# Kernel tuning notes

Measured on AMD Instinct MI355X. Metric: run time of the kernel, lower is better.

## Reference

```python
import jax, jax.numpy as jnp
import numpy as np

N_NODES = 50000
N_EDGES = 800000
IN_DIM, HID_DIM, OUT_DIM = 128, 64, 64
NEG_SLOPE = 0.2


def setup_inputs() -> dict:
    key = jax.random.key(0)
    ks = jax.random.split(key, 9)
    return {
        "x": jax.random.normal(ks[0], (N_NODES, IN_DIM), dtype=jnp.float32),
        "edge_index": jax.random.randint(ks[1], (2, N_EDGES), 0, N_NODES, dtype=jnp.int64),
        "W1": jax.random.normal(ks[2], (IN_DIM, HID_DIM), dtype=jnp.float32) * 0.1,
        "a1_src": jax.random.normal(ks[3], (HID_DIM,), dtype=jnp.float32) * 0.1,
        "a1_dst": jax.random.normal(ks[4], (HID_DIM,), dtype=jnp.float32) * 0.1,
        "b1": jnp.zeros((HID_DIM,), dtype=jnp.float32),
        "W2": jax.random.normal(ks[5], (HID_DIM, OUT_DIM), dtype=jnp.float32) * 0.1,
        "a2_src": jax.random.normal(ks[6], (OUT_DIM,), dtype=jnp.float32) * 0.1,
        "a2_dst": jax.random.normal(ks[7], (OUT_DIM,), dtype=jnp.float32) * 0.1,
        "b2": jnp.zeros((OUT_DIM,), dtype=jnp.float32),
    }


def gat_conv(x, src, dst, W, a_src, a_dst, b, n_nodes):
    """Single-head GATConv (PyG semantics, self-loops already appended)."""
    h = x @ W                               # [N, D]
    s_src = h @ a_src                       # [N]
    s_dst = h @ a_dst                       # [N]
    e = s_src[src] + s_dst[dst]             # [E] edge logits
    e = jnp.where(e >= 0, e, NEG_SLOPE * e)  # leaky_relu(0.2)
    # softmax over incoming edges of each destination node (numerically stable)
    m = jax.ops.segment_max(e, dst, num_segments=n_nodes)   # [N]
    e = jnp.exp(e - m[dst])
    denom = jax.ops.segment_sum(e, dst, num_segments=n_nodes)
    alpha = e / denom[dst]                  # [E]
    out = jax.ops.segment_sum(alpha[:, None] * h[src], dst, num_segments=n_nodes)
    return out + b


def reference(x, edge_index, W1, a1_src, a1_dst, b1, W2, a2_src, a2_dst, b2):
    n = x.shape[0]
    loop = jnp.arange(n, dtype=edge_index.dtype)
    src = jnp.concatenate([edge_index[0], loop])  # add self loops (PyG default)
    dst = jnp.concatenate([edge_index[1], loop])
    h = jax.nn.relu(gat_conv(x, src, dst, W1, a1_src, a1_dst, b1, n))
    out = gat_conv(h, src, dst, W2, a2_src, a2_dst, b2, n)
    return out
```

## Files before the change

kernel.cpp:

```cpp
#include <hip/hip_runtime.h>
#include <hip/hip_fp16.h>

#define N_NODES 50000
#define N_EDGES 800000
#define NEG_SLOPE 0.2f
#define NBKT 196
#define EBLK 200
#define CHUNK 4000
#define GEMM_BLOCKS 782

__device__ __forceinline__ float leaky(float x) { return x >= 0.f ? x : NEG_SLOPE * x; }
__device__ __forceinline__ float readlane_f(float v, int i) {
    return __uint_as_float(__builtin_amdgcn_readlane(__float_as_uint(v), i));
}
__device__ __forceinline__ unsigned enc_f(float f) {
    unsigned u = __float_as_uint(f);
    return (int)u < 0 ? ~u : (u | 0x80000000u);
}
__device__ __forceinline__ float dec_f(unsigned e) {
    return __uint_as_float((int)e < 0 ? (e & 0x7FFFFFFFu) : ~e);
}

template <int K>
__device__ __forceinline__ void gemm_body(
    const float* __restrict__ x, const float* __restrict__ W,
    const float* __restrict__ a_src, const float* __restrict__ a_dst,
    __half* __restrict__ h, float* __restrict__ s_src, float* __restrict__ s_dst,
    float* __restrict__ bmax, unsigned* __restrict__ gmax_enc, int n)
{
    constexpr int BK = 32;
    __shared__ float Wl[BK][64];
    __shared__ float xt[BK][68];
    __shared__ float asl[64], adl[64];
    __shared__ float wm[4];

    int tid = threadIdx.x;
    if (tid < 64) { asl[tid] = a_src[tid]; adl[tid] = a_dst[tid]; }
    int tx = tid & 15, ty = tid >> 4;
    int row0 = blockIdx.x * 64;

    float acc[4][4] = {};

    for (int k0 = 0; k0 < K; k0 += BK) {
        __syncthreads();
        {
            const float4* Wg = (const float4*)&W[(size_t)k0 * 64];
            float4* Ws = (float4*)&Wl[0][0];
            Ws[tid]       = Wg[tid];
            Ws[tid + 256] = Wg[tid + 256];
        }
        #pragma unroll
        for (int it = 0; it < 2; ++it) {
            int idx = tid + it * 256;
            int r = idx >> 3, kq = idx & 7;
            int grow = row0 + r;
            float4 v = (grow < n) ? *(const float4*)&x[(size_t)grow * K + k0 + kq * 4]
                                  : make_float4(0.f, 0.f, 0.f, 0.f);
            xt[kq * 4 + 0][r] = v.x;
            xt[kq * 4 + 1][r] = v.y;
            xt[kq * 4 + 2][r] = v.z;
            xt[kq * 4 + 3][r] = v.w;
        }
        __syncthreads();

        #pragma unroll
        for (int kk = 0; kk < BK; ++kk) {
            float4 wv = *(const float4*)&Wl[kk][tx * 4];
            float4 xv = *(const float4*)&xt[kk][ty * 4];
            acc[0][0] += xv.x * wv.x; acc[0][1] += xv.x * wv.y; acc[0][2] += xv.x * wv.z; acc[0][3] += xv.x * wv.w;
            acc[1][0] += xv.y * wv.x; acc[1][1] += xv.y * wv.y; acc[1][2] += xv.y * wv.z; acc[1][3] += xv.y * wv.w;
            acc[2][0] += xv.z * wv.x; acc[2][1] += xv.z * wv.y; acc[2][2] += xv.z * wv.z; acc[2][3] += xv.z * wv.w;
            acc[3][0] += xv.w * wv.x; acc[3][1] += xv.w * wv.y; acc[3][2] += xv.w * wv.z; acc[3][3] += xv.w * wv.w;
        }
    }

    float wmax = -INFINITY;
    #pragma unroll
    for (int i = 0; i < 4; ++i) {
        int grow = row0 + ty * 4 + i;
        if (grow < n) {
            __half2 p0 = __floats2half2_rn(acc[i][0], acc[i][1]);
            __half2 p1 = __floats2half2_rn(acc[i][2], acc[i][3]);
            uint2 pk = make_uint2(*(unsigned*)&p0, *(unsigned*)&p1);
            *(uint2*)&h[(size_t)grow * 64 + tx * 4] = pk;
        }
        float s1 = acc[i][0] * asl[tx*4+0] + acc[i][1] * asl[tx*4+1]
                 + acc[i][2] * asl[tx*4+2] + acc[i][3] * asl[tx*4+3];
        float s2 = acc[i][0] * adl[tx*4+0] + acc[i][1] * adl[tx*4+1]
                 + acc[i][2] * adl[tx*4+2] + acc[i][3] * adl[tx*4+3];
        #pragma unroll
        for (int m = 1; m < 16; m <<= 1) {
            s1 += __shfl_xor(s1, m, 64);
            s2 += __shfl_xor(s2, m, 64);
        }
        if (grow < n) wmax = fmaxf(wmax, s1);
        if (tx == 0 && grow < n) { s_src[grow] = s1; s_dst[grow] = s2; }
    }
    wmax = fmaxf(wmax, __shfl_xor(wmax, 16, 64));
    wmax = fmaxf(wmax, __shfl_xor(wmax, 32, 64));
    if ((tid & 63) == 0) wm[tid >> 6] = wmax;
    __syncthreads();
    if (tid == 0) {
        float bm = fmaxf(fmaxf(wm[0], wm[1]), fmaxf(wm[2], wm[3]));
        if (bmax) bmax[blockIdx.x] = bm;
        else      atomicMax(gmax_enc, enc_f(bm));
    }
}

template <int K>
__global__ __launch_bounds__(256) void fused_gemm_p1(
    const float* __restrict__ x, const float* __restrict__ W,
    const float* __restrict__ a_src, const float* __restrict__ a_dst,
    __half* __restrict__ h, float* __restrict__ s_src, float* __restrict__ s_dst,
    float* __restrict__ bmax,
    const int* __restrict__ dst_, int* __restrict__ cnt, int n)
{
    if (blockIdx.x >= GEMM_BLOCKS) {
        __shared__ int bins[NBKT];
        int tid = threadIdx.x, b = blockIdx.x - GEMM_BLOCKS;
        if (tid < NBKT) bins[tid] = 0;
        __syncthreads();
        int e0 = b * CHUNK;
        for (int e = e0 + tid; e < e0 + CHUNK; e += 256)
            atomicAdd(&bins[dst_[e] >> 8], 1);
        __syncthreads();
        if (tid < NBKT) cnt[b * NBKT + tid] = bins[tid];
        return;
    }
    gemm_body<K>(x, W, a_src, a_dst, h, s_src, s_dst, bmax, nullptr, n);
}

template <int K>
__global__ __launch_bounds__(256) void gat_gemm_kernel(
    const float* __restrict__ x, const float* __restrict__ W,
    const float* __restrict__ a_src, const float* __restrict__ a_dst,
    __half* __restrict__ h, float* __restrict__ s_src, float* __restrict__ s_dst,
    unsigned* __restrict__ gmax_enc, int n)
{
    gemm_body<K>(x, W, a_src, a_dst, h, s_src, s_dst, nullptr, gmax_enc, n);
}

__global__ __launch_bounds__(256) void p23_fused(
    const int* __restrict__ cnt, int* __restrict__ btot,
    const float* __restrict__ bmax, unsigned* __restrict__ gmaxu,
    const int* __restrict__ src, const int* __restrict__ dst,
    unsigned* __restrict__ bkted)
{
    __shared__ int tmp[256];
    __shared__ int boffL[NBKT];
    __shared__ float fm[4];
    int b = blockIdx.x, tid = threadIdx.x;

    int total = 0, myoff = 0;
    if (tid < NBKT) {
        for (int bp = 0; bp < EBLK; ++bp) {
            int v = cnt[bp * NBKT + tid];
            total += v;
            if (bp < b) myoff += v;
        }
    }
    tmp[tid] = (tid < NBKT) ? total : 0;
    __syncthreads();
    for (int off = 1; off < 256; off <<= 1) {
        int a = (tid >= off) ? tmp[tid - off] : 0;
        __syncthreads();
        tmp[tid] += a;
        __syncthreads();
    }
    if (tid < NBKT) {
        int base = tmp[tid] - total;
        boffL[tid] = base + myoff;
        if (b == 0) btot[tid] = total;
    }
    __syncthreads();

    int e0 = b * CHUNK;
    for (int e = e0 + tid; e < e0 + CHUNK; e += 256) {
        int d = dst[e], s = src[e];
        int pos = atomicAdd(&boffL[d >> 8], 1);
        bkted[pos] = ((unsigned)(d & 255) << 16) | (unsigned)s;
    }

    if (b == 0) {
        float m = -INFINITY;
        for (int i = tid; i < GEMM_BLOCKS; i += 256) m = fmaxf(m, bmax[i]);
        #pragma unroll
        for (int off = 32; off; off >>= 1) m = fmaxf(m, __shfl_xor(m, off, 64));
        if ((tid & 63) == 0) fm[tid >> 6] = m;
        __syncthreads();
        if (tid == 0) {
            gmaxu[0] = enc_f(fmaxf(fmaxf(fm[0], fm[1]), fmaxf(fm[2], fm[3])));
            gmaxu[1] = 0;
        }
    }
}

__global__ __launch_bounds__(256) void p4_csr(
    const unsigned* __restrict__ bkted, const int* __restrict__ btot,
    int* __restrict__ row_off, int* __restrict__ csr_src)
{
    __shared__ int tmp[256];
    __shared__ int cur[256];
    __shared__ int s_beg, s_end;
    int j = blockIdx.x, tid = threadIdx.x;
    int v = (tid < NBKT) ? btot[tid] : 0;
    tmp[tid] = v; __syncthreads();
    for (int off = 1; off < 256; off <<= 1) {
        int a = (tid >= off) ? tmp[tid - off] : 0;
        __syncthreads();
        tmp[tid] += a;
        __syncthreads();
    }
    if (tid == j) { s_beg = tmp[tid] - v; s_end = tmp[tid]; }
    cur[tid] = 0;
    __syncthreads();
    int beg = s_beg, end = s_end;

    for (int e = beg + tid; e < end; e += 256)
        atomicAdd(&cur[bkted[e] >> 16], 1);
    __syncthreads();
    int c = cur[tid];
    tmp[tid] = c; __syncthreads();
    for (int off = 1; off < 256; off <<= 1) {
        int a = (tid >= off) ? tmp[tid - off] : 0;
        __syncthreads();
        tmp[tid] += a;
        __syncthreads();
    }
    int offx = tmp[tid] - c;
    int node = j * 256 + tid;
    if (node < N_NODES) row_off[node] = beg + offx;
    if (node == 0) row_off[N_NODES] = N_EDGES;
    __syncthreads();
    cur[tid] = offx;
    __syncthreads();
    for (int e = beg + tid; e < end; e += 256) {
        unsigned u = bkted[e];
        int pos = beg + atomicAdd(&cur[u >> 16], 1);
        csr_src[pos] = (int)(u & 0xFFFFu);
    }
}

template <bool RELU>
__global__ __launch_bounds__(256) void gat_node_kernel(
    const int* __restrict__ row_off, const int* __restrict__ csr_src,
    const float* __restrict__ s_src, const float* __restrict__ s_dst,
    const __half* __restrict__ h, const float* __restrict__ b,
    const unsigned* __restrict__ gmax_enc, float* __restrict__ out, int n)
{
    int row = blockIdx.x * 4 + (threadIdx.x >> 6);
    int lane = threadIdx.x & 63;
    if (row >= n) return;

    int beg = row_off[row], end = row_off[row + 1];
    int deg = end - beg;
    float sd = s_dst[row];
    float m = leaky(dec_f(*gmax_enc) + sd);
    float s_self = s_src[row];
    float hself = __half2float(h[(size_t)row * 64 + lane]);
    float wself = __expf(leaky(s_self + sd) - m);

    if (deg <= 32) {
        int mysrc = row;
        if (lane < deg) mysrc = csr_src[beg + lane];
        float my_s = s_src[mysrc];
        float hv[32];
        #pragma unroll
        for (int j = 0; j < 32; ++j) {
            int s = __builtin_amdgcn_readlane(mysrc, j);
            hv[j] = __half2float(h[(size_t)s * 64 + lane]);
        }
        float mylogit = (lane < deg) ? leaky(my_s + sd) : -INFINITY;
        float w64 = __expf(mylogit - m);
        float den = w64;
        #pragma unroll
        for (int off = 32; off; off >>= 1)
            den += __shfl_xor(den, off, 64);
        den += wself;

        float acc = wself * hself;
        #pragma unroll
        for (int j = 0; j < 32; ++j)
            acc += readlane_f(w64, j) * hv[j];

        float v = acc / den + b[lane];
        if (RELU) v = fmaxf(v, 0.f);
        out[(size_t)row * 64 + lane] = v;
        return;
    }

    int   mysrc   = row;
    float mylogit = -INFINITY;
    if (lane < deg) {
        mysrc = csr_src[beg + lane];
        mylogit = leaky(s_src[mysrc] + sd);
    }
    float w64 = __expf(mylogit - m);
    float den = w64;
    #pragma unroll
    for (int off = 32; off; off >>= 1)
        den += __shfl_xor(den, off, 64);
    den += wself;

    float acc = wself * hself;
    int d0 = deg < 64 ? deg : 64;
    int nb = (d0 + 15) & ~15;
    for (int i = 0; i < nb; i += 16) {
        float hv[16];
        #pragma unroll
        for (int j = 0; j < 16; ++j) {
            int s = __builtin_amdgcn_readlane(mysrc, i + j);
            hv[j] = __half2float(h[(size_t)s * 64 + lane]);
        }
        #pragma unroll
        for (int j = 0; j < 16; ++j)
            acc += readlane_f(w64, i + j) * hv[j];
    }
    for (int e = beg + 64; e < end; ++e) {
        int s = csr_src[e];
        float w = __expf(leaky(s_src[s] + sd) - m);
        den += w;
        acc += w * __half2float(h[(size_t)s * 64 + lane]);
    }

    float v = acc / den + b[lane];
    if (RELU) v = fmaxf(v, 0.f);
    out[(size_t)row * 64 + lane] = v;
}

extern "C" void kernel_launch(void* const* d_in, const int* in_sizes, int n_in,
                              void* d_out, int out_size, void* d_ws, size_t ws_size,
                              hipStream_t stream) {
    const float* x   = (const float*)d_in[0];
    const int*   ei  = (const int*)d_in[1];
    const float* W1  = (const float*)d_in[2];
    const float* a1s = (const float*)d_in[3];
    const float* a1d = (const float*)d_in[4];
    const float* b1  = (const float*)d_in[5];
    const float* W2  = (const float*)d_in[6];
    const float* a2s = (const float*)d_in[7];
    const float* a2d = (const float*)d_in[8];
    const float* b2  = (const float*)d_in[9];
    float* out = (float*)d_out;

    const int* src = ei;
    const int* dst = ei + N_EDGES;

    char* p = (char*)d_ws;
    __half* h   = (__half*)p;           p += (size_t)N_NODES * 64 * 2;
    float* ssrc = (float*)p;            p += (size_t)N_NODES * 4;
    float* sdst = (float*)p;            p += (size_t)N_NODES * 4;
    int* row_off = (int*)p;             p += (size_t)(N_NODES + 1) * 4;
    unsigned* gmaxu = (unsigned*)p;     p += 4 * 4;
    float* bmax = (float*)p;            p += 1024 * 4;
    int* csr_src = (int*)p;             p += (size_t)N_EDGES * 4;
    int* cnt     = (int*)p;             p += (size_t)EBLK * NBKT * 4;
    int* btot    = (int*)p;             p += (size_t)NBKT * 4;
    unsigned* bkted = (unsigned*)p;     p += (size_t)N_EDGES * 4;

    dim3 blk(256);
    int node_blocks = (N_NODES + 3) / 4;

    fused_gemm_p1<128><<<GEMM_BLOCKS + EBLK, blk, 0, stream>>>(
        x, W1, a1s, a1d, h, ssrc, sdst, bmax, dst, cnt, N_NODES);
    p23_fused<<<EBLK, blk, 0, stream>>>(cnt, btot, bmax, gmaxu, src, dst, bkted);
    p4_csr<<<NBKT, blk, 0, stream>>>(bkted, btot, row_off, csr_src);
    gat_node_kernel<true><<<node_blocks, blk, 0, stream>>>(
        row_off, csr_src, ssrc, sdst, h, b1, gmaxu + 0, out, N_NODES);
    gat_gemm_kernel<64><<<GEMM_BLOCKS, blk, 0, stream>>>(
        out, W2, a2s, a2d, h, ssrc, sdst, gmaxu + 1, N_NODES);
    gat_node_kernel<false><<<node_blocks, blk, 0, stream>>>(
        row_off, csr_src, ssrc, sdst, h, b2, gmaxu + 1, out, N_NODES);
}
```

Measured before the change: 125.8 us.

## Fuse layer-1 aggregation with layer-2 GEMM in one node kernel

Merges the first GAT aggregation kernel with the second layer's dense transform. Each wavefront computes its aggregated row, applies ReLU, and multiplies by W2 held in shared memory using readlane broadcasts. It then writes h2, the attention scores and the block max directly, so the fp32 hidden activation never goes to global memory and one launch is removed. It also adds a 16-neighbour gather path for low-degree rows. The cost is separate h2/score buffers and a 64-step serial readlane matvec per row, along with a 16 KB W2 load per block.

Result: slower. 229.8 us (+82.7%).

```diff
diff --git a/kernel.cpp b/kernel.cpp
--- a/kernel.cpp
+++ b/kernel.cpp
@@ -21,12 +21,29 @@
     return __uint_as_float((int)e < 0 ? (e & 0x7FFFFFFFu) : ~e);
 }
 
+template <int NL>
+__device__ __forceinline__ float salvo(int mysrc, float w64,
+                                       const __half* __restrict__ h,
+                                       int lane, float acc)
+{
+    float hv[NL];
+    #pragma unroll
+    for (int j = 0; j < NL; ++j) {
+        int s = __builtin_amdgcn_readlane(mysrc, j);
+        hv[j] = __half2float(h[(size_t)s * 64 + lane]);
+    }
+    #pragma unroll
+    for (int j = 0; j < NL; ++j)
+        acc += readlane_f(w64, j) * hv[j];
+    return acc;
+}
+
 template <int K>
 __device__ __forceinline__ void gemm_body(
     const float* __restrict__ x, const float* __restrict__ W,
     const float* __restrict__ a_src, const float* __restrict__ a_dst,
     __half* __restrict__ h, float* __restrict__ s_src, float* __restrict__ s_dst,
-    float* __restrict__ bmax, unsigned* __restrict__ gmax_enc, int n)
+    float* __restrict__ bmax, int n)
 {
     constexpr int BK = 32;
     __shared__ float Wl[BK][64];
@@ -100,11 +117,8 @@
     wmax = fmaxf(wmax, __shfl_xor(wmax, 32, 64));
     if ((tid & 63) == 0) wm[tid >> 6] = wmax;
     __syncthreads();
-    if (tid == 0) {
-        float bm = fmaxf(fmaxf(wm[0], wm[1]), fmaxf(wm[2], wm[3]));
-        if (bmax) bmax[blockIdx.x] = bm;
-        else      atomicMax(gmax_enc, enc_f(bm));
-    }
+    if (tid == 0)
+        bmax[blockIdx.x] = fmaxf(fmaxf(wm[0], wm[1]), fmaxf(wm[2], wm[3]));
 }
 
 template <int K>
@@ -127,17 +141,7 @@
         if (tid < NBKT) cnt[b * NBKT + tid] = bins[tid];
         return;
     }
-    gemm_body<K>(x, W, a_src, a_dst, h, s_src, s_dst, bmax, nullptr, n);
-}
-
-template <int K>
-__global__ __launch_bounds__(256) void gat_gemm_kernel(
-    const float* __restrict__ x, const float* __restrict__ W,
-    const float* __restrict__ a_src, const float* __restrict__ a_dst,
-    __half* __restrict__ h, float* __restrict__ s_src, float* __restrict__ s_dst,
-    unsigned* __restrict__ gmax_enc, int n)
-{
-    gemm_body<K>(x, W, a_src, a_dst, h, s_src, s_dst, nullptr, gmax_enc, n);
+    gemm_body<K>(x, W, a_src, a_dst, h, s_src, s_dst, bmax, n);
 }
 
 __global__ __launch_bounds__(256) void p23_fused(
@@ -241,53 +245,19 @@
     }
 }
 
-template <bool RELU>
-__global__ __launch_bounds__(256) void gat_node_kernel(
+__device__ __forceinline__ float aggregate_row(
+    int row, int lane,
     const int* __restrict__ row_off, const int* __restrict__ csr_src,
     const float* __restrict__ s_src, const float* __restrict__ s_dst,
-    const __half* __restrict__ h, const float* __restrict__ b,
-    const unsigned* __restrict__ gmax_enc, float* __restrict__ out, int n)
-{
-    int row = blockIdx.x * 4 + (threadIdx.x >> 6);
-    int lane = threadIdx.x & 63;
-    if (row >= n) return;
-
+    const __half* __restrict__ h, const float* __restrict__ bvec,
+    float m_base)
+{
     int beg = row_off[row], end = row_off[row + 1];
     int deg = end - beg;
     float sd = s_dst[row];
-    float m = leaky(dec_f(*gmax_enc) + sd);
-    float s_self = s_src[row];
+    float m = leaky(m_base + sd);
     float hself = __half2float(h[(size_t)row * 64 + lane]);
-    float wself = __expf(leaky(s_self + sd) - m);
-
-    if (deg <= 32) {
-        int mysrc = row;
-        if (lane < deg) mysrc = csr_src[beg + lane];
-        float my_s = s_src[mysrc];
-        float hv[32];
-        #pragma unroll
-        for (int j = 0; j < 32; ++j) {
-            int s = __builtin_amdgcn_readlane(mysrc, j);
-            hv[j] = __half2float(h[(size_t)s * 64 + lane]);
-        }
-        float mylogit = (lane < deg) ? leaky(my_s + sd) : -INFINITY;
-        float w64 = __expf(mylogit - m);
-        float den = w64;
-        #pragma unroll
-        for (int off = 32; off; off >>= 1)
-            den += __shfl_xor(den, off, 64);
-        den += wself;
-
-        float acc = wself * hself;
-        #pragma unroll
-        for (int j = 0; j < 32; ++j)
-            acc += readlane_f(w64, j) * hv[j];
-
-        float v = acc / den + b[lane];
-        if (RELU) v = fmaxf(v, 0.f);
-        out[(size_t)row * 64 + lane] = v;
-        return;
-    }
+    float wself = __expf(leaky(s_src[row] + sd) - m);
 
     int   mysrc   = row;
     float mylogit = -INFINITY;
@@ -303,28 +273,116 @@
     den += wself;
 
     float acc = wself * hself;
-    int d0 = deg < 64 ? deg : 64;
-    int nb = (d0 + 15) & ~15;
-    for (int i = 0; i < nb; i += 16) {
-        float hv[16];
+
+    if (deg <= 16) {
+        acc = salvo<16>(mysrc, w64, h, lane, acc);
+    } else if (deg <= 32) {
+        acc = salvo<32>(mysrc, w64, h, lane, acc);
+    } else {
+        int d0 = deg < 64 ? deg : 64;
+        int nb = (d0 + 15) & ~15;
+        for (int i = 0; i < nb; i += 16) {
+            float hv[16];
+            #pragma unroll
+            for (int j = 0; j < 16; ++j) {
+                int s = __builtin_amdgcn_readlane(mysrc, i + j);
+                hv[j] = __half2float(h[(size_t)s * 64 + lane]);
+            }
+            #pragma unroll
+            for (int j = 0; j < 16; ++j)
+                acc += readlane_f(w64, i + j) * hv[j];
+        }
+        for (int e = beg + 64; e < end; ++e) {
+            int s = csr_src[e];
+            float w = __expf(leaky(s_src[s] + sd) - m);
+            den += w;
+            acc += w * __half2float(h[(size_t)s * 64 + lane]);
+        }
+    }
+    return acc / den + bvec[lane];
+}
+
+__global__ __launch_bounds__(256) void node1_gemm2_kernel(
+    const int* __restrict__ row_off, const int* __restrict__ csr_src,
+    const float* __restrict__ s_src, const float* __restrict__ s_dst,
+    const __half* __restrict__ h, const float* __restrict__ b1,
+    const float* __restrict__ W2,
+    const float* __restrict__ a2s, const float* __restrict__ a2d,
+    const unsigned* __restrict__ gmax1_enc, unsigned* __restrict__ gmax2_enc,
+    __half* __restrict__ h2, float* __restrict__ s_src2, float* __restrict__ s_dst2,
+    int n)
+{
+    __shared__ float W2l[64][64];
+    __shared__ float b1l[64], a2sl[64], a2dl[64];
+    __shared__ float wm[4];
+
+    int tid = threadIdx.x;
+    {
+        const float4* Wg = (const float4*)W2;
+        float4* Ws = (float4*)&W2l[0][0];
         #pragma unroll
-        for (int j = 0; j < 16; ++j) {
-            int s = __builtin_amdgcn_readlane(mysrc, i + j);
-            hv[j] = __half2float(h[(size_t)s * 64 + lane]);
-        }
-        #pragma unroll
-        for (int j = 0; j < 16; ++j)
-            acc += readlane_f(w64, i + j) * hv[j];
-    }
-    for (int e = beg + 64; e < end; ++e) {
-        int s = csr_src[e];
-        float w = __expf(leaky(s_src[s] + sd) - m);
-        den += w;
-        acc += w * __half2float(h[(size_t)s * 64 + lane]);
-    }
-
-    float v = acc / den + b[lane];
-    if (RELU) v = fmaxf(v, 0.f);
+        for (int it = 0; it < 4; ++it)
+            Ws[tid + it * 256] = Wg[tid + it * 256];
+        if (tid < 64) { b1l[tid] = b1[tid]; a2sl[tid] = a2s[tid]; a2dl[tid] = a2d[tid]; }
+    }
+    __syncthreads();
+
+    int row = blockIdx.x * 4 + (tid >> 6);
+    int lane = tid & 63;
+    float m_base = dec_f(*gmax1_enc);
+
+    float v = 0.f;
+    if (row < n) {
+        v = aggregate_row(row, lane, row_off, csr_src, s_src, s_dst, h, b1l, m_base);
+        v = fmaxf(v, 0.f);
+    }
+
+    float acc2 = 0.f;
+    #pragma unroll 8
+    for (int k = 0; k < 64; ++k) {
+        float vk = readlane_f(v, k);
+        acc2 += vk * W2l[k][lane];
+    }
+
+    float s1 = acc2 * a2sl[lane];
+    float s2 = acc2 * a2dl[lane];
+    #pragma unroll
+    for (int off = 1; off < 64; off <<= 1) {
+        s1 += __shfl_xor(s1, off, 64);
+        s2 += __shfl_xor(s2, off, 64);
+    }
+
+    if (row < n) {
+        h2[(size_t)row * 64 + lane] = __float2half(acc2);
+        if (lane == 0) { s_src2[row] = s1; s_dst2[row] = s2; }
+    }
+
+    float wmax = (row < n) ? s1 : -INFINITY;
+    if ((tid & 63) == 0) wm[tid >> 6] = wmax;
+    __syncthreads();
+    if (tid == 0) {
+        float bm = fmaxf(fmaxf(wm[0], wm[1]), fmaxf(wm[2], wm[3]));
+        atomicMax(gmax2_enc, enc_f(bm));
+    }
+}
+
+__global__ __launch_bounds__(256) void gat_node_kernel(
+    const int* __restrict__ row_off, const int* __restrict__ csr_src,
+    const float* __restrict__ s_src, const float* __restrict__ s_dst,
+    const __half* __restrict__ h, const float* __restrict__ b,
+    const unsigned* __restrict__ gmax_enc, float* __restrict__ out, int n)
+{
+    __shared__ float bl[64];
+    int tid = threadIdx.x;
+    if (tid < 64) bl[tid] = b[tid];
+    __syncthreads();
+
+    int row = blockIdx.x * 4 + (tid >> 6);
+    int lane = tid & 63;
+    if (row >= n) return;
+
+    float v = aggregate_row(row, lane, row_off, csr_src, s_src, s_dst, h, bl,
+                            dec_f(*gmax_enc));
     out[(size_t)row * 64 + lane] = v;
 }
 
@@ -348,8 +406,11 @@
 
     char* p = (char*)d_ws;
     __half* h   = (__half*)p;           p += (size_t)N_NODES * 64 * 2;
+    __half* h2  = (__half*)p;           p += (size_t)N_NODES * 64 * 2;
     float* ssrc = (float*)p;            p += (size_t)N_NODES * 4;
     float* sdst = (float*)p;            p += (size_t)N_NODES * 4;
+    float* ssrc2 = (float*)p;           p += (size_t)N_NODES * 4;
+    float* sdst2 = (float*)p;           p += (size_t)N_NODES * 4;
     int* row_off = (int*)p;             p += (size_t)(N_NODES + 1) * 4;
     unsigned* gmaxu = (unsigned*)p;     p += 4 * 4;
     float* bmax = (float*)p;            p += 1024 * 4;
@@ -365,10 +426,9 @@
         x, W1, a1s, a1d, h, ssrc, sdst, bmax, dst, cnt, N_NODES);
     p23_fused<<<EBLK, blk, 0, stream>>>(cnt, btot, bmax, gmaxu, src, dst, bkted);
     p4_csr<<<NBKT, blk, 0, stream>>>(bkted, btot, row_off, csr_src);
-    gat_node_kernel<true><<<node_blocks, blk, 0, stream>>>(
-        row_off, csr_src, ssrc, sdst, h, b1, gmaxu + 0, out, N_NODES);
-    gat_gemm_kernel<64><<<GEMM_BLOCKS, blk, 0, stream>>>(
-        out, W2, a2s, a2d, h, ssrc, sdst, gmaxu + 1, N_NODES);
-    gat_node_kernel<false><<<node_blocks, blk, 0, stream>>>(
-        row_off, csr_src, ssrc, sdst, h, b2, gmaxu + 1, out, N_NODES);
-}
+    node1_gemm2_kernel<<<node_blocks, blk, 0, stream>>>(
+        row_off, csr_src, ssrc, sdst, h, b1, W2, a2s, a2d,
+        gmaxu + 0, gmaxu + 1, h2, ssrc2, sdst2, N_NODES);
+    gat_node_kernel<<<node_blocks, blk, 0, stream>>>(
+        row_off, csr_src, ssrc2, sdst2, h2, b2, gmaxu + 1, out, N_NODES);
+}
```
